# Kernel optimization log

Hardware: AMD Instinct MI355X
Metric: run time of the kernel (lower is better)

## Reference

```python
import jax, jax.numpy as jnp
import numpy as np

B = 16384
D_VIS, D_LANG, D_STATE = 768, 768, 64
D = 256          # d_model
E = 4            # n_experts
K = 2            # top_k
D_IN = D_VIS + D_LANG + D_STATE
EPS = 1e-5


def layernorm(x, g, b):
    mu = x.mean(-1, keepdims=True)
    var = ((x - mu) ** 2).mean(-1, keepdims=True)
    return g * (x - mu) / jnp.sqrt(var + EPS) + b


def setup_inputs() -> dict:
    key = jax.random.key(0)
    ks = jax.random.split(key, 16)
    s = 0.02
    return {
        "vis": jax.random.normal(ks[0], (B, D_VIS), jnp.float32),
        "lang": jax.random.normal(ks[1], (B, D_LANG), jnp.float32),
        "state": jax.random.normal(ks[2], (B, D_STATE), jnp.float32),
        # fusion: Linear(d_in, d_model) + LayerNorm
        "Wf": jax.random.normal(ks[3], (D_IN, D), jnp.float32) * s,
        "bf": jnp.zeros((D,), jnp.float32),
        "gf": jnp.ones((D,), jnp.float32),
        "bfln": jnp.zeros((D,), jnp.float32),
        # gate (bias=False); random instead of zeros so routing is nontrivial
        "Wg": jax.random.normal(ks[4], (D, E), jnp.float32) * s,
        # stacked experts: Linear(d,2d) -> GELU -> Linear(2d,d) -> GELU -> Linear(d,d), then LN(x + net(x))
        "W1": jax.random.normal(ks[5], (E, D, 2 * D), jnp.float32) * s,
        "b1": jnp.zeros((E, 2 * D), jnp.float32),
        "W2": jax.random.normal(ks[6], (E, 2 * D, D), jnp.float32) * s,
        "b2": jnp.zeros((E, D), jnp.float32),
        "W3": jax.random.normal(ks[7], (E, D, D), jnp.float32) * s,
        "b3": jnp.zeros((E, D), jnp.float32),
        "eg": jnp.ones((E, D), jnp.float32),
        "eb": jnp.zeros((E, D), jnp.float32),
    }


def reference(vis, lang, state, Wf, bf, gf, bfln, Wg, W1, b1, W2, b2, W3, b3, eg, eb):
    gelu = lambda t: jax.nn.gelu(t, approximate=False)
    # fusion: Linear -> LayerNorm -> GELU  (dropout is eval-mode identity)
    x = jnp.concatenate([vis, lang, state], axis=-1) @ Wf + bf   # [B, D]
    x = gelu(layernorm(x, gf, bfln))

    logits = x @ Wg                                              # [B, E]
    all_probs = jax.nn.softmax(logits, axis=-1)
    top_vals, top_idx = jax.lax.top_k(logits, K)                 # [B, K]
    top_w = jax.nn.softmax(top_vals, axis=-1)                    # [B, K]

    # all experts densely (E small); original computes same math per masked subset
    h = gelu(jnp.einsum('bd,edh->beh', x, W1) + b1)              # [B, E, 2D]
    h = gelu(jnp.einsum('beh,ehd->bed', h, W2) + b2)             # [B, E, D]
    h = jnp.einsum('bed,edf->bef', h, W3) + b3                   # [B, E, D]
    y = layernorm(x[:, None, :] + h, eg, eb)                     # [B, E, D]

    # gather selected experts and combine with top-k weights
    y_sel = jnp.take_along_axis(y, top_idx[:, :, None], axis=1)  # [B, K, D]
    out = jnp.einsum('bk,bkd->bd', top_w, y_sel)                 # [B, D]

    # load-balance loss: importance x load
    counts = jnp.zeros((E,), x.dtype).at[top_idx.reshape(-1)].add(1.0)
    f_i = counts / (B * K)
    lb_loss = E * jnp.sum(f_i * all_probs.mean(0))
    return out, lb_loss
```

## Files before the change

kernel.cpp:

```cpp
#include <hip/hip_runtime.h>
#include <math.h>


typedef unsigned short u16;
typedef unsigned int u32;
typedef __attribute__((ext_vector_type(8))) short bf16x8;
typedef __attribute__((ext_vector_type(4))) float f32x4;

__device__ __forceinline__ float bf2f(u16 u) {
    union { u32 i; float f; } v; v.i = ((u32)u) << 16; return v.f;
}
__device__ __forceinline__ u16 f2bf(float f) {
    union { float f; u32 i; } v; v.f = f;
    u32 x = v.i;
    return (u16)((x + 0x7fffu + ((x >> 16) & 1u)) >> 16);
}
__device__ __forceinline__ float gelu_exact(float v) {
    return 0.5f * v * (1.0f + erff(v * 0.70710678118654752f));
}

typedef __attribute__((address_space(1))) void GV;
typedef __attribute__((address_space(3))) void SV;
__device__ __forceinline__ void gldlds(const void* g, void* l) {
    __builtin_amdgcn_global_load_lds((GV*)g, (SV*)l, 16, 0, 0);
}

__device__ __forceinline__ u32 pk2(u32 f0, u32 f1) {
    return __builtin_amdgcn_perm(f1, f0, 0x07060302);
}

__device__ __forceinline__ void stageA64_R32(const u16* Ag, int lda, u16* As, int tid) {
    int s = tid;
    int m = s >> 3, c = s & 7;
    gldlds(Ag + m * lda + (c ^ (m & 7)) * 8, As + s * 8);
}
__device__ __forceinline__ void stageB64(const u16* Bg, int ldb, u16* Bs, int tid) {
#pragma unroll
    for (int i = 0; i < 8; ++i) {
        int s = i * 256 + tid;
        int n = s >> 3, c = s & 7;
        gldlds(Bg + n * ldb + (c ^ (n & 7)) * 8, Bs + s * 8);
    }
}
__device__ __forceinline__ void compute64_R32(const u16* As, const u16* Bs, f32x4 acc[2][4],
                                              int w, int l16, int quad) {
#pragma unroll
    for (int ks = 0; ks < 2; ++ks) {
        bf16x8 a[2];
#pragma unroll
        for (int mt = 0; mt < 2; ++mt) {
            int m = mt * 16 + l16;
            a[mt] = *(const bf16x8*)(As + m * 64 + (((ks * 4 + quad) ^ (m & 7)) << 3));
        }
#pragma unroll
        for (int nt = 0; nt < 4; ++nt) {
            int n = w * 64 + nt * 16 + l16;
            bf16x8 b = *(const bf16x8*)(Bs + n * 64 + (((ks * 4 + quad) ^ (n & 7)) << 3));
#pragma unroll
            for (int mt = 0; mt < 2; ++mt)
                acc[mt][nt] = __builtin_amdgcn_mfma_f32_16x16x32_bf16(a[mt], b, acc[mt][nt], 0, 0, 0);
        }
    }
}
__device__ __forceinline__ void stageA128_512(const u16* Ag, int lda, u16* As, int tid) {
#pragma unroll
    for (int i = 0; i < 2; ++i) {
        int s = i * 512 + tid;
        int m = s >> 3, c = s & 7;
        gldlds(Ag + m * lda + (c ^ (m & 7)) * 8, As + s * 8);
    }
}
__device__ __forceinline__ void stageB64_512(const u16* Bg, int ldb, u16* Bs, int tid) {
#pragma unroll
    for (int i = 0; i < 4; ++i) {
        int s = i * 512 + tid;
        int n = s >> 3, c = s & 7;
        gldlds(Bg + n * ldb + (c ^ (n & 7)) * 8, Bs + s * 8);
    }
}
__device__ __forceinline__ void compute128_8w(const u16* As, const u16* Bs, f32x4 acc[4][4],
                                              int wrw, int wc, int l16, int quad) {
#pragma unroll
    for (int ks = 0; ks < 2; ++ks) {
        bf16x8 a[4];
#pragma unroll
        for (int mt = 0; mt < 4; ++mt) {
            int m = wrw * 64 + mt * 16 + l16;
            a[mt] = *(const bf16x8*)(As + m * 64 + (((ks * 4 + quad) ^ (m & 7)) << 3));
        }
#pragma unroll
        for (int nt = 0; nt < 4; ++nt) {
            int n = wc * 64 + nt * 16 + l16;
            bf16x8 b = *(const bf16x8*)(Bs + n * 64 + (((ks * 4 + quad) ^ (n & 7)) << 3));
#pragma unroll
            for (int mt = 0; mt < 4; ++mt)
                acc[mt][nt] = __builtin_amdgcn_mfma_f32_16x16x32_bf16(a[mt], b, acc[mt][nt], 0, 0, 0);
        }
    }
}

#define SEG_WF  409600
#define SEG_W1  524288
#define SEG_W2  524288
#define SEG_W3  262144
#define PREP_ITEMS (SEG_WF + SEG_W1 + SEG_W2 + SEG_W3 + 8)

__global__ __launch_bounds__(256) void prep_kernel(
    const float* __restrict__ Wf, const float* __restrict__ W1, const float* __restrict__ W2,
    const float* __restrict__ W3,
    u16* __restrict__ wft, u16* __restrict__ w1t, u16* __restrict__ w2t, u16* __restrict__ w3t,
    float* __restrict__ lbacc) {
    int idx = blockIdx.x * 256 + threadIdx.x;
    if (idx < SEG_WF) {
        int n = idx / 1600, k = idx % 1600;
        wft[idx] = f2bf(Wf[(size_t)k * 256 + n]);
        return;
    }
    idx -= SEG_WF;
    if (idx < SEG_W1) {
        int e = idx >> 17, r = idx & 131071;
        int n = r >> 8, k = r & 255;
        w1t[idx] = f2bf(W1[(size_t)e * 131072 + (size_t)k * 512 + n]);
        return;
    }
    idx -= SEG_W1;
    if (idx < SEG_W2) {
        int e = idx >> 17, r = idx & 131071;
        int n = r >> 9, k = r & 511;
        w2t[idx] = f2bf(W2[(size_t)e * 131072 + (size_t)k * 256 + n]);
        return;
    }
    idx -= SEG_W2;
    if (idx < SEG_W3) {
        int e = idx >> 16, r = idx & 65535;
        int n = r >> 8, k = r & 255;
        w3t[idx] = f2bf(W3[(size_t)e * 65536 + (size_t)k * 256 + n]);
        return;
    }
    idx -= SEG_W3;
    if (idx < 8) lbacc[idx] = 0.0f;
}

__global__ __launch_bounds__(512, 4) void fusion_kernel(
    const float* __restrict__ vis, const float* __restrict__ lang, const float* __restrict__ state,
    const u16* __restrict__ BT, const float* __restrict__ bfv_, const float* __restrict__ gf,
    const float* __restrict__ bfln, const float* __restrict__ Wg,
    u16* __restrict__ xbf, float* __restrict__ wr, float* __restrict__ lbacc) {
    __shared__ __align__(16) u32 Af[4096];
    __shared__ __align__(16) u16 Bs[16384];
    int tid = threadIdx.x;
    int w = tid >> 6, lane = tid & 63, quad = lane >> 4, l16 = lane & 15;
    int wrw = w >> 2, wc = w & 3;
    int m0 = blockIdx.x * 64;
    f32x4 acc[2][4] = {};

    for (int kit = 0; kit < 25; ++kit) {
        const float* base; int ld;
        if (kit < 12)      { base = vis   + (size_t)m0 * 768 + kit * 64;        ld = 768; }
        else if (kit < 24) { base = lang  + (size_t)m0 * 768 + (kit - 12) * 64; ld = 768; }
        else               { base = state + (size_t)m0 * 64;                    ld = 64; }
#pragma unroll
        for (int i = 0; i < 2; ++i) {
            int s = i * 512 + tid;
            int m = s >> 4, c = s & 15;
            gldlds(base + m * ld + (c ^ (m & 15)) * 4, Af + s * 4);
        }
        stageB64_512(BT + kit * 64, 1600, Bs, tid);
        __syncthreads();
#pragma unroll
        for (int ks = 0; ks < 2; ++ks) {
            bf16x8 a[2];
#pragma unroll
            for (int mt = 0; mt < 2; ++mt) {
                int m = wrw * 32 + mt * 16 + l16;
                int c0 = ks * 8 + quad * 2;
                const u32* rowp = Af + m * 64;
                uint4 f0 = *(const uint4*)(rowp + (c0 ^ (m & 15)) * 4);
                uint4 f1 = *(const uint4*)(rowp + ((c0 + 1) ^ (m & 15)) * 4);
                union { u32 u[4]; bf16x8 v; } pk;
                pk.u[0] = pk2(f0.x, f0.y); pk.u[1] = pk2(f0.z, f0.w);
                pk.u[2] = pk2(f1.x, f1.y); pk.u[3] = pk2(f1.z, f1.w);
                a[mt] = pk.v;
            }
#pragma unroll
            for (int nt = 0; nt < 4; ++nt) {
                int n = wc * 64 + nt * 16 + l16;
                bf16x8 b = *(const bf16x8*)(Bs + n * 64 + (((ks * 4 + quad) ^ (n & 7)) << 3));
#pragma unroll
                for (int mt = 0; mt < 2; ++mt)
                    acc[mt][nt] = __builtin_amdgcn_mfma_f32_16x16x32_bf16(a[mt], b, acc[mt][nt], 0, 0, 0);
            }
        }
        __syncthreads();
    }

    float2* red  = (float2*)Af;
    float*  muv  = (float*)(Af + 512);
    float*  rsv  = (float*)(Af + 576);
    float*  gred = (float*)(Af + 640);
    float*  sacc = (float*)(Af + 1664);

    float bv[4], gvv[4], blv[4]; float4 wgv[4];
#pragma unroll
    for (int nt = 0; nt < 4; ++nt) {
        int col = wc * 64 + nt * 16 + l16;
        bv[nt] = bfv_[col]; gvv[nt] = gf[col]; blv[nt] = bfln[col];
        wgv[nt] = *(const float4*)(Wg + col * 4);
    }
    if (tid < 8) sacc[tid] = 0.f;
#pragma unroll
    for (int mt = 0; mt < 2; ++mt)
#pragma unroll
        for (int r = 0; r < 4; ++r) {
            float ss = 0.f, qq = 0.f;
#pragma unroll
            for (int nt = 0; nt < 4; ++nt) {
                float v = acc[mt][nt][r] + bv[nt];
                acc[mt][nt][r] = v;
                ss += v; qq += v * v;
            }
#pragma unroll
            for (int d = 1; d < 16; d <<= 1) { ss += __shfl_xor(ss, d); qq += __shfl_xor(qq, d); }
            if (l16 == 0) red[w * 32 + mt * 16 + quad * 4 + r] = make_float2(ss, qq);
        }
    __syncthreads();
    if (tid < 64) {
        int wrh = tid >> 5, rl2 = tid & 31;
        float ss = 0.f, qq = 0.f;
#pragma unroll
        for (int ww = 0; ww < 4; ++ww) {
            float2 t = red[(wrh * 4 + ww) * 32 + rl2]; ss += t.x; qq += t.y;
        }
        float mu = ss * (1.f / 256.f);
        float var = qq * (1.f / 256.f) - mu * mu;
        muv[tid] = mu;
        rsv[tid] = 1.f / sqrtf(var + 1e-5f);
    }
    __syncthreads();
#pragma unroll
    for (int mt = 0; mt < 2; ++mt)
#pragma unroll
        for (int r = 0; r < 4; ++r) {
            int rl2 = mt * 16 + quad * 4 + r;
            int row = wrw * 32 + rl2;
            float mu = muv[row], rs = rsv[row];
#pragma unroll
            for (int nt = 0; nt < 4; ++nt) {
                int col = wc * 64 + nt * 16 + l16;
                float t = (acc[mt][nt][r] - mu) * rs * gvv[nt] + blv[nt];
                float g = gelu_exact(t);
                acc[mt][nt][r] = g;
                xbf[(size_t)(m0 + row) * 256 + col] = f2bf(g);
            }
        }
#pragma unroll
    for (int mt = 0; mt < 2; ++mt)
#pragma unroll
        for (int r = 0; r < 4; ++r) {
            int rl2 = mt * 16 + quad * 4 + r;
            float p0 = 0.f, p1 = 0.f, p2 = 0.f, p3 = 0.f;
#pragma unroll
            for (int nt = 0; nt < 4; ++nt) {
                float g = acc[mt][nt][r];
                p0 += g * wgv[nt].x; p1 += g * wgv[nt].y;
                p2 += g * wgv[nt].z; p3 += g * wgv[nt].w;
            }
#pragma unroll
            for (int d = 1; d < 16; d <<= 1) {
                p0 += __shfl_xor(p0, d); p1 += __shfl_xor(p1, d);
                p2 += __shfl_xor(p2, d); p3 += __shfl_xor(p3, d);
            }
            if (l16 == 0) {
                float* gp = gred + w * 128 + rl2 * 4;
                gp[0] = p0; gp[1] = p1; gp[2] = p2; gp[3] = p3;
            }
        }
    __syncthreads();
    if (tid < 64) {
        int row = tid, wrh = row >> 5, rl2 = row & 31;
        float lg[4];
#pragma unroll
        for (int e = 0; e < 4; ++e) {
            float s = 0.f;
#pragma unroll
            for (int ww = 0; ww < 4; ++ww) s += gred[(wrh * 4 + ww) * 128 + rl2 * 4 + e];
            lg[e] = s;
        }
        float mx = fmaxf(fmaxf(lg[0], lg[1]), fmaxf(lg[2], lg[3]));
        float ex[4]; float Z = 0.f;
#pragma unroll
        for (int e = 0; e < 4; ++e) { ex[e] = expf(lg[e] - mx); Z += ex[e]; }
        int i0 = 0; float v0 = lg[0];
#pragma unroll
        for (int e = 1; e < 4; ++e) if (lg[e] > v0) { v0 = lg[e]; i0 = e; }
        int i1 = -1; float v1 = -1e30f;
#pragma unroll
        for (int e = 0; e < 4; ++e) if (e != i0 && lg[e] > v1) { v1 = lg[e]; i1 = e; }
        float t = expf(v1 - v0);
        float wA = 1.f / (1.f + t), wB = t / (1.f + t);
        float w4[4] = {0.f, 0.f, 0.f, 0.f};
        w4[i0] = wA; w4[i1] = wB;
#pragma unroll
        for (int e = 0; e < 4; ++e) wr[(size_t)(m0 + row) * 4 + e] = w4[e];
#pragma unroll
        for (int e = 0; e < 4; ++e) atomicAdd(&sacc[e], ex[e] / Z);
        atomicAdd(&sacc[4 + i0], 1.f);
        atomicAdd(&sacc[4 + i1], 1.f);
    }
    __syncthreads();
    if (tid < 8) atomicAdd(lbacc + tid, sacc[tid]);
}

__global__ __launch_bounds__(512, 4) void expert_gemm_kernel(
    const u16* __restrict__ A, int lda, size_t aE,
    const u16* __restrict__ BT, size_t bE,
    const float* __restrict__ bias, int biasE,
    u16* __restrict__ outp, int ldo, size_t oE) {
    __shared__ __align__(16) u16 As[8192];
    __shared__ __align__(16) u16 Bs[16384];
    int tid = threadIdx.x;
    int w = tid >> 6, lane = tid & 63, quad = lane >> 4, l16 = lane & 15;
    int wrw = w >> 2, wc = w & 3;
    int m0 = blockIdx.x * 128;
    int col0 = blockIdx.y * 256;
    int e = blockIdx.z;
    f32x4 acc[4][4] = {};
    const u16* Ag = A + e * aE + (size_t)m0 * lda;
    const u16* Bg = BT + e * bE + (size_t)col0 * lda;
    int kiters = lda >> 6;
    for (int kit = 0; kit < kiters; ++kit) {
        stageA128_512(Ag + kit * 64, lda, As, tid);
        stageB64_512(Bg + kit * 64, lda, Bs, tid);
        __syncthreads();
        compute128_8w(As, Bs, acc, wrw, wc, l16, quad);
        __syncthreads();
    }
#pragma unroll
    for (int nt = 0; nt < 4; ++nt) {
        int col = col0 + wc * 64 + nt * 16 + l16;
        float bvv = bias[e * biasE + col];
#pragma unroll
        for (int mt = 0; mt < 4; ++mt)
#pragma unroll
            for (int r = 0; r < 4; ++r) {
                int row = m0 + wrw * 64 + mt * 16 + quad * 4 + r;
                outp[e * oE + (size_t)row * ldo + col] = f2bf(gelu_exact(acc[mt][nt][r] + bvv));
            }
    }
}

__global__ __launch_bounds__(256) void combine_kernel(
    const u16* __restrict__ h2, const u16* __restrict__ W3T,
    const float* __restrict__ b3, const float* __restrict__ eg, const float* __restrict__ eb,
    const u16* __restrict__ xbf, const float* __restrict__ wr,
    const float* __restrict__ lbacc, float* __restrict__ outp) {
    __shared__ __align__(16) u16 As[2048];
    __shared__ __align__(16) u16 Bs[16384];
    __shared__ __align__(16) u16 xs[8192];
    __shared__ float wl[128];
    int tid = threadIdx.x;
    int w = tid >> 6, lane = tid & 63, quad = lane >> 4, l16 = lane & 15;
    int m0 = blockIdx.x * 32;
    if (blockIdx.x == 0 && tid == 0) {
        float lb = 0.f;
#pragma unroll
        for (int e = 0; e < 4; ++e)
            lb += (lbacc[4 + e] / 32768.f) * (lbacc[e] / 16384.f);
        outp[4194304] = 4.f * lb;
    }
#pragma unroll
    for (int i = 0; i < 4; ++i) {
        int s = i * 256 + tid;
        *(uint4*)(xs + s * 8) = *(const uint4*)(xbf + (size_t)m0 * 256 + s * 8);
    }
    if (tid < 128) wl[tid] = wr[(size_t)m0 * 4 + tid];
    float2* red = (float2*)As;
    float* muv = (float*)((char*)As + 1024);
    float* rsv = (float*)((char*)As + 1152);
    f32x4 oacc[2][4] = {};
    for (int e = 0; e < 4; ++e) {
        __syncthreads();
        f32x4 acc[2][4] = {};
        const u16* Ag = h2 + ((size_t)e * 16384 + m0) * 256;
        const u16* Bg = W3T + (size_t)e * 65536;
        for (int kit = 0; kit < 4; ++kit) {
            stageA64_R32(Ag + kit * 64, 256, As, tid);
            stageB64(Bg + kit * 64, 256, Bs, tid);
            __syncthreads();
            compute64_R32(As, Bs, acc, w, l16, quad);
            __syncthreads();
        }
        float b3v[4], egv[4], ebv[4];
#pragma unroll
        for (int nt = 0; nt < 4; ++nt) {
            int col = w * 64 + nt * 16 + l16;
            b3v[nt] = b3[e * 256 + col]; egv[nt] = eg[e * 256 + col]; ebv[nt] = eb[e * 256 + col];
        }
#pragma unroll
        for (int mt = 0; mt < 2; ++mt)
#pragma unroll
            for (int r = 0; r < 4; ++r) {
                int rl = mt * 16 + quad * 4 + r;
                float ss = 0.f, qq = 0.f;
#pragma unroll
                for (int nt = 0; nt < 4; ++nt) {
                    int col = w * 64 + nt * 16 + l16;
                    float v = acc[mt][nt][r] + b3v[nt] + bf2f(xs[rl * 256 + col]);
                    acc[mt][nt][r] = v;
                    ss += v; qq += v * v;
                }
#pragma unroll
                for (int d = 1; d < 16; d <<= 1) { ss += __shfl_xor(ss, d); qq += __shfl_xor(qq, d); }
                if (l16 == 0) red[w * 32 + rl] = make_float2(ss, qq);
            }
        __syncthreads();
        if (tid < 32) {
            float ss = 0.f, qq = 0.f;
#pragma unroll
            for (int ww = 0; ww < 4; ++ww) { float2 t = red[ww * 32 + tid]; ss += t.x; qq += t.y; }
            float mu = ss * (1.f / 256.f);
            float var = qq * (1.f / 256.f) - mu * mu;
            muv[tid] = mu;
            rsv[tid] = 1.f / sqrtf(var + 1e-5f);
        }
        __syncthreads();
#pragma unroll
        for (int mt = 0; mt < 2; ++mt)
#pragma unroll
            for (int r = 0; r < 4; ++r) {
                int rl = mt * 16 + quad * 4 + r;
                float mu = muv[rl], rs = rsv[rl], we = wl[rl * 4 + e];
#pragma unroll
                for (int nt = 0; nt < 4; ++nt) {
                    float y = (acc[mt][nt][r] - mu) * rs * egv[nt] + ebv[nt];
                    oacc[mt][nt][r] += we * y;
                }
            }
    }
#pragma unroll
    for (int mt = 0; mt < 2; ++mt)
#pragma unroll
        for (int r = 0; r < 4; ++r) {
            int rl = mt * 16 + quad * 4 + r;
#pragma unroll
            for (int nt = 0; nt < 4; ++nt) {
                int col = w * 64 + nt * 16 + l16;
                outp[(size_t)(m0 + rl) * 256 + col] = oacc[mt][nt][r];
            }
        }
}

extern "C" void kernel_launch(void* const* d_in, const int* in_sizes, int n_in,
                              void* d_out, int out_size, void* d_ws, size_t ws_size,
                              hipStream_t stream) {
    const float* vis   = (const float*)d_in[0];
    const float* lang  = (const float*)d_in[1];
    const float* state = (const float*)d_in[2];
    const float* Wf    = (const float*)d_in[3];
    const float* bf_   = (const float*)d_in[4];
    const float* gf    = (const float*)d_in[5];
    const float* bfln  = (const float*)d_in[6];
    const float* Wg    = (const float*)d_in[7];
    const float* W1    = (const float*)d_in[8];
    const float* b1    = (const float*)d_in[9];
    const float* W2    = (const float*)d_in[10];
    const float* b2    = (const float*)d_in[11];
    const float* W3    = (const float*)d_in[12];
    const float* b3    = (const float*)d_in[13];
    const float* eg    = (const float*)d_in[14];
    const float* eb    = (const float*)d_in[15];
    float* outp = (float*)d_out;

    char* ws = (char*)d_ws;
    size_t off = 0;
    float* lbacc = (float*)(ws + off); off += 256;
    u16* WFT  = (u16*)(ws + off); off += 819200UL;
    u16* W1T  = (u16*)(ws + off); off += 1048576UL;
    u16* W2T  = (u16*)(ws + off); off += 1048576UL;
    u16* W3T  = (u16*)(ws + off); off += 524288UL;
    u16* XBF  = (u16*)(ws + off); off += 8388608UL;
    float* WR = (float*)(ws + off); off += 262144UL;
    u16* H1   = (u16*)(ws + off); off += 67108864UL;
    u16* H2   = (u16*)(ws + off); off += 33554432UL;
    if (ws_size < off) return;

    int prep_blocks = (PREP_ITEMS + 255) / 256;
    prep_kernel<<<prep_blocks, 256, 0, stream>>>(Wf, W1, W2, W3, WFT, W1T, W2T, W3T, lbacc);
    fusion_kernel<<<256, 512, 0, stream>>>(vis, lang, state, WFT, bf_, gf, bfln, Wg,
                                           XBF, WR, lbacc);
    expert_gemm_kernel<<<dim3(128, 2, 4), 512, 0, stream>>>(
        XBF, 256, 0, W1T, 131072, b1, 512, H1, 512, 8388608UL);
    expert_gemm_kernel<<<dim3(128, 1, 4), 512, 0, stream>>>(
        H1, 512, 8388608UL, W2T, 131072, b2, 256, H2, 256, 4194304UL);
    combine_kernel<<<512, 256, 0, stream>>>(H2, W3T, b3, eg, eb, XBF, WR, lbacc, outp);
}
```

Before: 319.1 us.

## Split fusion GEMM over K into two halves and use tiled transposes in prep

The fusion GEMM now runs on a 256x2 grid, with each half of the K range written as fp32 partials into the H1 workspace. A new epilogue kernel sums the partials, adds the bias, and applies LayerNorm, GELU, the gate logits and routing. With only 256 blocks before, the GPU was underfilled, so the split is meant to double the block count. The cost is an extra 32 MB round trip of partials plus one more launch. Separately, the weight-prep transpose now goes through a 32x32 shared-memory tile, so both its reads and its writes are coalesced instead of strided.

```diff
diff --git a/kernel.cpp b/kernel.cpp
--- a/kernel.cpp
+++ b/kernel.cpp
@@ -98,63 +98,52 @@
         }
     }
 }
-
-#define SEG_WF  409600
-#define SEG_W1  524288
-#define SEG_W2  524288
-#define SEG_W3  262144
-#define PREP_ITEMS (SEG_WF + SEG_W1 + SEG_W2 + SEG_W3 + 8)
 
 __global__ __launch_bounds__(256) void prep_kernel(
     const float* __restrict__ Wf, const float* __restrict__ W1, const float* __restrict__ W2,
     const float* __restrict__ W3,
     u16* __restrict__ wft, u16* __restrict__ w1t, u16* __restrict__ w2t, u16* __restrict__ w3t,
     float* __restrict__ lbacc) {
-    int idx = blockIdx.x * 256 + threadIdx.x;
-    if (idx < SEG_WF) {
-        int n = idx / 1600, k = idx % 1600;
-        wft[idx] = f2bf(Wf[(size_t)k * 256 + n]);
-        return;
-    }
-    idx -= SEG_WF;
-    if (idx < SEG_W1) {
-        int e = idx >> 17, r = idx & 131071;
-        int n = r >> 8, k = r & 255;
-        w1t[idx] = f2bf(W1[(size_t)e * 131072 + (size_t)k * 512 + n]);
-        return;
-    }
-    idx -= SEG_W1;
-    if (idx < SEG_W2) {
-        int e = idx >> 17, r = idx & 131071;
-        int n = r >> 9, k = r & 511;
-        w2t[idx] = f2bf(W2[(size_t)e * 131072 + (size_t)k * 256 + n]);
-        return;
-    }
-    idx -= SEG_W2;
-    if (idx < SEG_W3) {
-        int e = idx >> 16, r = idx & 65535;
-        int n = r >> 8, k = r & 255;
-        w3t[idx] = f2bf(W3[(size_t)e * 65536 + (size_t)k * 256 + n]);
-        return;
-    }
-    idx -= SEG_W3;
-    if (idx < 8) lbacc[idx] = 0.0f;
-}
-
-__global__ __launch_bounds__(512, 4) void fusion_kernel(
+    int b = blockIdx.x;
+    int tid = threadIdx.x;
+    const float* src; u16* dst; int K, N, kt, ntl;
+    if (b < 400)      { src = Wf; dst = wft; K = 1600; N = 256; kt = b % 50; ntl = b / 50; }
+    else if (b < 912) { int r = b - 400, e = r >> 7; r &= 127;
+                        src = W1 + (size_t)e * 131072; dst = w1t + (size_t)e * 131072;
+                        K = 256; N = 512; kt = r & 7; ntl = r >> 3; }
+    else if (b < 1424){ int r = b - 912, e = r >> 7; r &= 127;
+                        src = W2 + (size_t)e * 131072; dst = w2t + (size_t)e * 131072;
+                        K = 512; N = 256; kt = r & 15; ntl = r >> 4; }
+    else if (b < 1680){ int r = b - 1424, e = r >> 6; r &= 63;
+                        src = W3 + (size_t)e * 65536; dst = w3t + (size_t)e * 65536;
+                        K = 256; N = 256; kt = r & 7; ntl = r >> 3; }
+    else { if (tid < 8) lbacc[tid] = 0.0f; return; }
+    int k0 = kt * 32, n0 = ntl * 32;
+    __shared__ float tl[32][33];
+    int j = tid & 31, i0 = (tid >> 5) << 2;
+#pragma unroll
+    for (int ii = 0; ii < 4; ++ii)
+        tl[i0 + ii][j] = src[(size_t)(k0 + i0 + ii) * N + n0 + j];
+    __syncthreads();
+#pragma unroll
+    for (int ii = 0; ii < 4; ++ii)
+        dst[(size_t)(n0 + i0 + ii) * K + k0 + j] = f2bf(tl[j][i0 + ii]);
+}
+
+__global__ __launch_bounds__(512, 4) void fusion_gemm_kernel(
     const float* __restrict__ vis, const float* __restrict__ lang, const float* __restrict__ state,
-    const u16* __restrict__ BT, const float* __restrict__ bfv_, const float* __restrict__ gf,
-    const float* __restrict__ bfln, const float* __restrict__ Wg,
-    u16* __restrict__ xbf, float* __restrict__ wr, float* __restrict__ lbacc) {
+    const u16* __restrict__ BT, float* __restrict__ P) {
     __shared__ __align__(16) u32 Af[4096];
     __shared__ __align__(16) u16 Bs[16384];
     int tid = threadIdx.x;
     int w = tid >> 6, lane = tid & 63, quad = lane >> 4, l16 = lane & 15;
     int wrw = w >> 2, wc = w & 3;
     int m0 = blockIdx.x * 64;
+    int khalf = blockIdx.y;
+    int kbeg = khalf ? 12 : 0, kend = khalf ? 25 : 12;
     f32x4 acc[2][4] = {};
 
-    for (int kit = 0; kit < 25; ++kit) {
+    for (int kit = kbeg; kit < kend; ++kit) {
         const float* base; int ld;
         if (kit < 12)      { base = vis   + (size_t)m0 * 768 + kit * 64;        ld = 768; }
         else if (kit < 24) { base = lang  + (size_t)m0 * 768 + (kit - 12) * 64; ld = 768; }
@@ -193,99 +182,71 @@
         }
         __syncthreads();
     }
-
-    float2* red  = (float2*)Af;
-    float*  muv  = (float*)(Af + 512);
-    float*  rsv  = (float*)(Af + 576);
-    float*  gred = (float*)(Af + 640);
-    float*  sacc = (float*)(Af + 1664);
-
-    float bv[4], gvv[4], blv[4]; float4 wgv[4];
-#pragma unroll
-    for (int nt = 0; nt < 4; ++nt) {
-        int col = wc * 64 + nt * 16 + l16;
-        bv[nt] = bfv_[col]; gvv[nt] = gf[col]; blv[nt] = bfln[col];
-        wgv[nt] = *(const float4*)(Wg + col * 4);
-    }
-    if (tid < 8) sacc[tid] = 0.f;
 #pragma unroll
     for (int mt = 0; mt < 2; ++mt)
 #pragma unroll
         for (int r = 0; r < 4; ++r) {
-            float ss = 0.f, qq = 0.f;
-#pragma unroll
-            for (int nt = 0; nt < 4; ++nt) {
-                float v = acc[mt][nt][r] + bv[nt];
-                acc[mt][nt][r] = v;
-                ss += v; qq += v * v;
-            }
-#pragma unroll
-            for (int d = 1; d < 16; d <<= 1) { ss += __shfl_xor(ss, d); qq += __shfl_xor(qq, d); }
-            if (l16 == 0) red[w * 32 + mt * 16 + quad * 4 + r] = make_float2(ss, qq);
-        }
-    __syncthreads();
-    if (tid < 64) {
-        int wrh = tid >> 5, rl2 = tid & 31;
-        float ss = 0.f, qq = 0.f;
-#pragma unroll
-        for (int ww = 0; ww < 4; ++ww) {
-            float2 t = red[(wrh * 4 + ww) * 32 + rl2]; ss += t.x; qq += t.y;
-        }
-        float mu = ss * (1.f / 256.f);
-        float var = qq * (1.f / 256.f) - mu * mu;
-        muv[tid] = mu;
-        rsv[tid] = 1.f / sqrtf(var + 1e-5f);
-    }
-    __syncthreads();
-#pragma unroll
-    for (int mt = 0; mt < 2; ++mt)
-#pragma unroll
-        for (int r = 0; r < 4; ++r) {
-            int rl2 = mt * 16 + quad * 4 + r;
-            int row = wrw * 32 + rl2;
-            float mu = muv[row], rs = rsv[row];
+            int row = wrw * 32 + mt * 16 + quad * 4 + r;
 #pragma unroll
             for (int nt = 0; nt < 4; ++nt) {
                 int col = wc * 64 + nt * 16 + l16;
-                float t = (acc[mt][nt][r] - mu) * rs * gvv[nt] + blv[nt];
-                float g = gelu_exact(t);
-                acc[mt][nt][r] = g;
-                xbf[(size_t)(m0 + row) * 256 + col] = f2bf(g);
-            }
-        }
-#pragma unroll
-    for (int mt = 0; mt < 2; ++mt)
-#pragma unroll
-        for (int r = 0; r < 4; ++r) {
-            int rl2 = mt * 16 + quad * 4 + r;
-            float p0 = 0.f, p1 = 0.f, p2 = 0.f, p3 = 0.f;
-#pragma unroll
-            for (int nt = 0; nt < 4; ++nt) {
-                float g = acc[mt][nt][r];
-                p0 += g * wgv[nt].x; p1 += g * wgv[nt].y;
-                p2 += g * wgv[nt].z; p3 += g * wgv[nt].w;
-            }
-#pragma unroll
-            for (int d = 1; d < 16; d <<= 1) {
-                p0 += __shfl_xor(p0, d); p1 += __shfl_xor(p1, d);
-                p2 += __shfl_xor(p2, d); p3 += __shfl_xor(p3, d);
-            }
-            if (l16 == 0) {
-                float* gp = gred + w * 128 + rl2 * 4;
-                gp[0] = p0; gp[1] = p1; gp[2] = p2; gp[3] = p3;
-            }
-        }
+                P[((size_t)khalf * 16384 + m0 + row) * 256 + col] = acc[mt][nt][r];
+            }
+        }
+}
+
+__global__ __launch_bounds__(256) void fusion_epi_kernel(
+    const float* __restrict__ P, const float* __restrict__ bfv_, const float* __restrict__ gf,
+    const float* __restrict__ bfln, const float* __restrict__ Wg,
+    u16* __restrict__ xbf, float* __restrict__ wr, float* __restrict__ lbacc) {
+    __shared__ float sacc[8];
+    int tid = threadIdx.x;
+    int m0 = blockIdx.x * 32;
+    int row = tid >> 3;
+    int cs = (tid & 7) * 32;
+    if (tid < 8) sacc[tid] = 0.f;
+    const float* p0 = P + ((size_t)(m0 + row)) * 256 + cs;
+    const float* p1 = P + ((size_t)(16384 + m0 + row)) * 256 + cs;
+    float v[32];
+    float ss = 0.f, qq = 0.f;
+#pragma unroll
+    for (int j = 0; j < 32; j += 4) {
+        float4 a = *(const float4*)(p0 + j);
+        float4 b = *(const float4*)(p1 + j);
+        float4 bb = *(const float4*)(bfv_ + cs + j);
+        v[j + 0] = a.x + b.x + bb.x; v[j + 1] = a.y + b.y + bb.y;
+        v[j + 2] = a.z + b.z + bb.z; v[j + 3] = a.w + b.w + bb.w;
+        ss += v[j] + v[j + 1] + v[j + 2] + v[j + 3];
+        qq += v[j] * v[j] + v[j + 1] * v[j + 1] + v[j + 2] * v[j + 2] + v[j + 3] * v[j + 3];
+    }
+#pragma unroll
+    for (int d = 1; d < 8; d <<= 1) { ss += __shfl_xor(ss, d); qq += __shfl_xor(qq, d); }
+    float mu = ss * (1.f / 256.f);
+    float var = qq * (1.f / 256.f) - mu * mu;
+    float rs = 1.f / sqrtf(var + 1e-5f);
+    float pe0 = 0.f, pe1 = 0.f, pe2 = 0.f, pe3 = 0.f;
+#pragma unroll
+    for (int j = 0; j < 32; ++j) {
+        float t = (v[j] - mu) * rs * gf[cs + j] + bfln[cs + j];
+        float g = gelu_exact(t);
+        v[j] = g;
+        float4 wg = *(const float4*)(Wg + (cs + j) * 4);
+        pe0 += g * wg.x; pe1 += g * wg.y; pe2 += g * wg.z; pe3 += g * wg.w;
+    }
+    u16* xp = xbf + (size_t)(m0 + row) * 256 + cs;
+#pragma unroll
+    for (int j = 0; j < 32; j += 2) {
+        u32 wv = (u32)f2bf(v[j]) | ((u32)f2bf(v[j + 1]) << 16);
+        *(u32*)(xp + j) = wv;
+    }
+#pragma unroll
+    for (int d = 1; d < 8; d <<= 1) {
+        pe0 += __shfl_xor(pe0, d); pe1 += __shfl_xor(pe1, d);
+        pe2 += __shfl_xor(pe2, d); pe3 += __shfl_xor(pe3, d);
+    }
     __syncthreads();
-    if (tid < 64) {
-        int row = tid, wrh = row >> 5, rl2 = row & 31;
-        float lg[4];
-#pragma unroll
-        for (int e = 0; e < 4; ++e) {
-            float s = 0.f;
-#pragma unroll
-            for (int ww = 0; ww < 4; ++ww) s += gred[(wrh * 4 + ww) * 128 + rl2 * 4 + e];
-            lg[e] = s;
-        }
+    if ((tid & 7) == 0) {
+        float lg[4] = {pe0, pe1, pe2, pe3};
         float mx = fmaxf(fmaxf(lg[0], lg[1]), fmaxf(lg[2], lg[3]));
         float ex[4]; float Z = 0.f;
 #pragma unroll
@@ -483,11 +444,11 @@
     u16* H1   = (u16*)(ws + off); off += 67108864UL;
     u16* H2   = (u16*)(ws + off); off += 33554432UL;
     if (ws_size < off) return;
-
-    int prep_blocks = (PREP_ITEMS + 255) / 256;
-    prep_kernel<<<prep_blocks, 256, 0, stream>>>(Wf, W1, W2, W3, WFT, W1T, W2T, W3T, lbacc);
-    fusion_kernel<<<256, 512, 0, stream>>>(vis, lang, state, WFT, bf_, gf, bfln, Wg,
-                                           XBF, WR, lbacc);
+    float* P = (float*)H1;
+
+    prep_kernel<<<1681, 256, 0, stream>>>(Wf, W1, W2, W3, WFT, W1T, W2T, W3T, lbacc);
+    fusion_gemm_kernel<<<dim3(256, 2), 512, 0, stream>>>(vis, lang, state, WFT, P);
+    fusion_epi_kernel<<<512, 256, 0, stream>>>(P, bf_, gf, bfln, Wg, XBF, WR, lbacc);
     expert_gemm_kernel<<<dim3(128, 2, 4), 512, 0, stream>>>(
         XBF, 256, 0, W1T, 131072, b1, 512, H1, 512, 8388608UL);
     expert_gemm_kernel<<<dim3(128, 1, 4), 512, 0, stream>>>(
```

Result: slower. 332.1 us (+4.1%).
